# Performance work log

Measured on AMD Instinct MI355X. Metric: run time of the kernel, lower is better.

Reference implementation:

```python
import jax, jax.numpy as jnp
import numpy as np

EPS = 1e-6
N_HEADS, N_KV = 16, 4


def rmsnorm(x, w):
    return x * jax.lax.rsqrt(jnp.mean(x * x, axis=-1, keepdims=True) + EPS) * w


def setup_inputs() -> dict:
    key = jax.random.key(0)
    ks = jax.random.split(key, 9)
    B, T, D, F = 2, 2048, 2048, 8192
    KVD = N_KV * (D // N_HEADS)
    s = lambda k, shape, fan: (jax.random.normal(k, shape, jnp.float32) * (fan ** -0.5))
    return {
        "x": jax.random.normal(ks[0], (B, T, D), jnp.float32),
        "norm1_w": jnp.ones((D,), jnp.float32),
        "norm2_w": jnp.ones((D,), jnp.float32),
        "Wq": s(ks[1], (D, D), D),
        "Wk": s(ks[2], (D, KVD), D),
        "Wv": s(ks[3], (D, KVD), D),
        "Wo": s(ks[4], (D, D), D),
        "Wc": s(ks[5], (D, D), D),
        "W1": s(ks[6], (D, F), D),
        "W2": s(ks[7], (F, D), F),
        "W3": s(ks[8], (D, F), D),
    }


def reference(x, norm1_w, norm2_w, Wq, Wk, Wv, Wo, Wc, W1, W2, W3):
    B, T, D = x.shape
    dh = D // N_HEADS          # 128
    G = N_HEADS // N_KV        # groups per kv head
    scale = dh ** -0.5

    xn = rmsnorm(x, norm1_w)
    q = xn @ Wq                               # [B,T,D]
    pos = q @ Wc                              # CoPE stand-in: contextual positional bias on Q
    q = (q + pos).reshape(B, T, N_KV, G, dh)  # group q heads under their kv head
    k = (xn @ Wk).reshape(B, T, N_KV, dh)
    v = (xn @ Wv).reshape(B, T, N_KV, dh)

    # GQA without repeat_interleave: contract each group against shared K/V
    scores = jnp.einsum('bqkgd,bskd->bkgqs', q, k) * scale   # [B,KV,G,T,T]
    i = jnp.arange(T)
    causal = i[:, None] >= i[None, :]
    scores = jnp.where(causal, scores, -jnp.inf)
    w = jax.nn.softmax(scores, axis=-1)
    att = jnp.einsum('bkgqs,bskd->bqkgd', w, v).reshape(B, T, D)

    x = x + att @ Wo
    xn2 = rmsnorm(x, norm2_w)
    x = x + (jax.nn.silu(xn2 @ W1) * (xn2 @ W3)) @ W2
    return x
```

## Files before the change

### kernel.cpp

```cpp
#include <hip/hip_runtime.h>
#include <hip/hip_bf16.h>

typedef __attribute__((ext_vector_type(8))) short short8;
typedef __attribute__((ext_vector_type(4))) float floatx4;
typedef unsigned short ushort_t;

__device__ inline float b2f(ushort_t s) {
    return __uint_as_float(((unsigned int)s) << 16);
}
__device__ inline ushort_t f2b(float f) {
    unsigned int u = __float_as_uint(f);
    unsigned int r = 0x7fff + ((u >> 16) & 1);
    return (ushort_t)((u + r) >> 16);
}
__device__ inline void load8(const float* p, float* f) {
    float4 a = *(const float4*)p;
    float4 b = *(const float4*)(p + 4);
    f[0] = a.x; f[1] = a.y; f[2] = a.z; f[3] = a.w;
    f[4] = b.x; f[5] = b.y; f[6] = b.z; f[7] = b.w;
}
__device__ inline void gload16(const ushort_t* g, ushort_t* l) {
    __builtin_amdgcn_global_load_lds(
        (const __attribute__((address_space(1))) unsigned int*)g,
        (__attribute__((address_space(3))) unsigned int*)l, 16, 0, 0);
}

__global__ __launch_bounds__(256) void transpose_w(const float* __restrict__ src,
                                                   ushort_t* __restrict__ dst,
                                                   int K, int N) {
    __shared__ ushort_t tile[64][65];
    int kb = blockIdx.x * 64, nb = blockIdx.y * 64;
    int t = threadIdx.x;
#pragma unroll
    for (int i = 0; i < 4; ++i) {
        int r = (t >> 4) + i * 16;
        int c = (t & 15) * 4;
        float4 v = *(const float4*)(src + (size_t)(kb + r) * N + nb + c);
        tile[c + 0][r] = f2b(v.x);
        tile[c + 1][r] = f2b(v.y);
        tile[c + 2][r] = f2b(v.z);
        tile[c + 3][r] = f2b(v.w);
    }
    __syncthreads();
#pragma unroll
    for (int i = 0; i < 2; ++i) {
        int s = t + i * 256;
        int n = s >> 3, kc = (s & 7) * 8;
        ushort_t o[8];
#pragma unroll
        for (int j = 0; j < 8; ++j) o[j] = tile[n][kc + j];
        *(uint4*)(dst + (size_t)(nb + n) * K + kb + kc) = *(const uint4*)o;
    }
}

__global__ __launch_bounds__(256) void rmsnorm_kernel(const float* __restrict__ x,
                                                      const float* __restrict__ w,
                                                      ushort_t* __restrict__ out, int D) {
    int row = blockIdx.x;
    int t = threadIdx.x;
    const float* xr = x + (size_t)row * D;
    float f[8];
    load8(xr + t * 8, f);
    float ss = 0.f;
#pragma unroll
    for (int i = 0; i < 8; ++i) ss += f[i] * f[i];
#pragma unroll
    for (int m = 1; m < 64; m <<= 1) ss += __shfl_xor(ss, m);
    __shared__ float wsum[4];
    if ((t & 63) == 0) wsum[t >> 6] = ss;
    __syncthreads();
    float tot = wsum[0] + wsum[1] + wsum[2] + wsum[3];
    float r = rsqrtf(tot / (float)D + 1e-6f);
    float wf[8];
    load8(w + t * 8, wf);
    ushort_t o[8];
#pragma unroll
    for (int i = 0; i < 8; ++i) o[i] = f2b(f[i] * r * wf[i]);
    *(uint4*)(out + (size_t)row * D + t * 8) = *(const uint4*)o;
}

__global__ __launch_bounds__(256) void reduce_out(const ushort_t* __restrict__ p,
                                                  const float* __restrict__ resid,
                                                  float* __restrict__ out, int n) {
    int stride = gridDim.x * 256;
    for (int i = blockIdx.x * 256 + threadIdx.x; i * 8 < n; i += stride) {
        int i8 = i * 8;
        uint4 a = *(const uint4*)(p + i8);
        uint4 b = *(const uint4*)(p + n + i8);
        const ushort_t* ae = (const ushort_t*)&a;
        const ushort_t* be = (const ushort_t*)&b;
        float rr[8];
        load8(resid + i8, rr);
        float o[8];
#pragma unroll
        for (int j = 0; j < 8; ++j) o[j] = b2f(ae[j]) + b2f(be[j]) + rr[j];
        *(float4*)(out + i8) = make_float4(o[0], o[1], o[2], o[3]);
        *(float4*)(out + i8 + 4) = make_float4(o[4], o[5], o[6], o[7]);
    }
}

__device__ inline void vm6() { asm volatile("s_waitcnt vmcnt(6)" ::: "memory"); }

template <int MODE>
__global__ __launch_bounds__(512, 2) void gemm8(const ushort_t* __restrict__ A,
                                                const ushort_t* __restrict__ Bt,
                                                const ushort_t* __restrict__ aux,
                                                const float* __restrict__ aux2,
                                                void* __restrict__ Cv,
                                                void* __restrict__ C2v,
                                                void* __restrict__ C3v,
                                                int M, int N, int Ksub, int lda) {
    __shared__ __align__(16) ushort_t Lds[2 * 32768];
    const int tid = threadIdx.x;
    const int wv = tid >> 6, lane = tid & 63;
    const int l16 = lane & 15, l4 = lane >> 4;
    const int wr = wv >> 2, wc = wv & 3;
    int nwg = gridDim.x;
    int per = nwg >> 3;
    int wg = (blockIdx.x & 7) * per + (blockIdx.x >> 3);
    int mtiles = M >> 8;
    int bx = wg & (mtiles - 1);
    int by = wg / mtiles;
    int bm = bx << 8, bn = by << 8;
    int koff = blockIdx.y * Ksub;

    const int sr = tid >> 3;
    const int scol = (((tid & 7) ^ (sr & 7)) << 3);
    const ushort_t* gA = A + (size_t)(bm + sr) * lda + scol + koff;
    const ushort_t* gB = Bt + (size_t)(bn + sr) * lda + scol + koff;
    ushort_t* ldsw = Lds + wv * 512;

    const int ktiles = Ksub >> 6;
    const int niter = ktiles >> 1;
    const int km = ktiles - 1;

#define STG_A(slot, j, kt) gload16(gA + (size_t)((j) * 64) * lda + ((kt) << 6), ldsw + (slot) * 32768 + (j) * 4096)
#define STG_B(slot, j, kt) gload16(gB + (size_t)((j) * 64) * lda + ((kt) << 6), ldsw + (slot) * 32768 + 16384 + (j) * 4096)

    STG_A(0, 0, 0); STG_A(0, 2, 0); STG_A(0, 1, 0); STG_A(0, 3, 0);
    STG_B(0, 0, 0); STG_B(0, 1, 0); STG_B(0, 2, 0); STG_B(0, 3, 0);
    STG_A(1, 0, 1); STG_A(1, 2, 1);
    STG_B(1, 0, 1); STG_B(1, 1, 1); STG_B(1, 2, 1); STG_B(1, 3, 1);
    vm6();
    asm volatile("" ::: "memory");
    __builtin_amdgcn_s_barrier();

    const int lx = l4 ^ (l16 & 7);
    floatx4 acc[8][4] = {};
    short8 aR[4][2], bR[4][2];

#define DSA(slot, mh) { _Pragma("unroll") for (int m = 0; m < 4; ++m) { \
    _Pragma("unroll") for (int kk = 0; kk < 2; ++kk) \
      aR[m][kk] = *(const short8*)(Lds + (slot) * 32768 + \
          (wr * 128 + (mh) * 64 + m * 16 + l16) * 64 + ((lx ^ (kk << 2)) << 3)); } }
#define DSB(slot, nh) { _Pragma("unroll") for (int n = 0; n < 2; ++n) { \
    _Pragma("unroll") for (int kk = 0; kk < 2; ++kk) \
      bR[(nh) * 2 + n][kk] = *(const short8*)(Lds + (slot) * 32768 + 16384 + \
          (wc * 64 + ((nh) * 2 + n) * 16 + l16) * 64 + ((lx ^ (kk << 2)) << 3)); } }
#define QUAD(mh, nlo) { _Pragma("unroll") for (int m = 0; m < 4; ++m) \
    _Pragma("unroll") for (int n = 0; n < 2; ++n) \
    _Pragma("unroll") for (int kk = 0; kk < 2; ++kk) \
      acc[(mh) * 4 + m][(nlo) + n] = __builtin_amdgcn_mfma_f32_16x16x32_bf16( \
          aR[m][kk], bR[(nlo) + n][kk], acc[(mh) * 4 + m][(nlo) + n], 0, 0, 0); }
#define PHASE(DS, ST, MH, NLO, VM) { \
    DS; ST; \
    asm volatile("" ::: "memory"); \
    __builtin_amdgcn_s_barrier(); \
    asm volatile("s_waitcnt lgkmcnt(0)" ::: "memory"); \
    __builtin_amdgcn_sched_barrier(0); \
    __builtin_amdgcn_s_setprio(1); \
    QUAD(MH, NLO); \
    __builtin_amdgcn_s_setprio(0); \
    VM; \
    asm volatile("" ::: "memory"); \
    __builtin_amdgcn_s_barrier(); }

    for (int it = 0; it < niter; ++it) {
        int t1 = 2 * it + 1;
        int t2 = (2 * it + 2) & km;
        int t3 = (2 * it + 3) & km;
        PHASE({ DSA(0, 0); DSB(0, 0); }, { STG_A(1, 1, t1); STG_A(1, 3, t1); }, 0, 0, );
        PHASE({ DSB(0, 1); },            { STG_A(0, 0, t2); STG_A(0, 2, t2); }, 0, 2, );
        PHASE({ DSA(0, 1); },            { STG_B(0, 0, t2); STG_B(0, 1, t2); }, 1, 2, );
        PHASE({ },                       { STG_B(0, 2, t2); STG_B(0, 3, t2); }, 1, 0, vm6(); );
        PHASE({ DSA(1, 0); DSB(1, 0); }, { STG_A(0, 1, t2); STG_A(0, 3, t2); }, 0, 0, );
        PHASE({ DSB(1, 1); },            { STG_A(1, 0, t3); STG_A(1, 2, t3); }, 0, 2, );
        PHASE({ DSA(1, 1); },            { STG_B(1, 0, t3); STG_B(1, 1, t3); }, 1, 2, );
        PHASE({ },                       { STG_B(1, 2, t3); STG_B(1, 3, t3); }, 1, 0, vm6(); );
    }

#pragma unroll
    for (int mi = 0; mi < 8; ++mi)
#pragma unroll
        for (int ni = 0; ni < 4; ++ni)
#pragma unroll
            for (int r = 0; r < 4; ++r) {
                int row = bm + wr * 128 + mi * 16 + l4 * 4 + r;
                int col = bn + wc * 64 + ni * 16 + l16;
                size_t idx = (size_t)row * N + col;
                float v = acc[mi][ni][r];
                if (MODE == 0) {
                    ((ushort_t*)Cv)[idx] = f2b(v);
                } else if (MODE == 1) {
                    ((ushort_t*)Cv)[idx] = f2b(v + b2f(aux[idx]));
                } else if (MODE == 2) {
                    float h = b2f(aux[idx]);
                    ((ushort_t*)Cv)[idx] = f2b((h / (1.f + __expf(-h))) * v);
                } else if (MODE == 3) {
                    ((ushort_t*)Cv)[(size_t)blockIdx.y * M * N + idx] = f2b(v);
                } else if (MODE == 5) {
                    ((float*)Cv)[idx] = v + aux2[idx];
                } else if (MODE == 6) {
                    if (bn < 2048) {
                        ((ushort_t*)Cv)[(size_t)row * 2048 + col] = f2b(v);
                    } else if (bn < 2560) {
                        ((ushort_t*)C2v)[(size_t)row * 512 + (col - 2048)] = f2b(v);
                    } else {
                        ((ushort_t*)C3v)[(size_t)(col - 2560) * 4096 + row] = f2b(v);
                    }
                }
            }
#undef STG_A
#undef STG_B
#undef DSA
#undef DSB
#undef QUAD
#undef PHASE
}

#define QB 64
#define SB 64

__global__ __launch_bounds__(256, 2) void attn_kernel(const ushort_t* __restrict__ Q,
                                                      const ushort_t* __restrict__ Kb,
                                                      const ushort_t* __restrict__ VbT,
                                                      ushort_t* __restrict__ O, int Tlen) {
    const int D = 2048, KVD = 512, dh = 128;
    const int MTOK = 4096;
    int p = blockIdx.x, h = blockIdx.y, b = blockIdx.z;
    int kv = h >> 2;
    int t = threadIdx.x, wave = t >> 6, lane = t & 63;
    int l16 = lane & 15, l4 = lane >> 4;
    __shared__ __align__(16) ushort_t Ks[SB][dh + 8];
    __shared__ __align__(16) ushort_t Vt[dh][SB + 8];
    __shared__ __align__(16) ushort_t Ps[4][16][SB + 8];
    const float scale = 0.08838834764831845f;
    const ushort_t* Kg = Kb + ((size_t)(b * Tlen) + (t >> 4)) * KVD + kv * dh + (t & 15) * 8;
    const ushort_t* Vg = VbT + (size_t)(kv * dh + (t >> 3)) * MTOK + b * Tlen + (t & 7) * 8;

    for (int side = 0; side < 2; ++side) {
        int qt = side ? p : (31 - p);
        int qbase = qt * QB;
        int qfrag = qbase + wave * 16;
        short8 qf[4];
        const ushort_t* Qrow = Q + ((size_t)(b * Tlen) + qfrag + l16) * D + h * dh;
#pragma unroll
        for (int kk = 0; kk < 4; ++kk) qf[kk] = *(const short8*)(Qrow + kk * 32 + l4 * 8);
        floatx4 o_acc[8] = {};
        float m_r[4], l_r[4];
#pragma unroll
        for (int r = 0; r < 4; ++r) { m_r[r] = -INFINITY; l_r[r] = 0.f; }
        int nst = qt + 1;
        uint4 kreg[4], vreg[4];
#pragma unroll
        for (int p4 = 0; p4 < 4; ++p4) {
            kreg[p4] = *(const uint4*)(Kg + (size_t)(p4 * 16) * KVD);
            vreg[p4] = *(const uint4*)(Vg + (size_t)(p4 * 32) * MTOK);
        }
        for (int st = 0; st < nst; ++st) {
            __syncthreads();
#pragma unroll
            for (int p4 = 0; p4 < 4; ++p4) {
                *(uint4*)(&Ks[(t >> 4) + p4 * 16][(t & 15) * 8]) = kreg[p4];
                *(uint4*)(&Vt[(t >> 3) + p4 * 32][(t & 7) * 8]) = vreg[p4];
            }
            __syncthreads();
            if (st + 1 < nst) {
                size_t off = (size_t)(st + 1) * SB;
#pragma unroll
                for (int p4 = 0; p4 < 4; ++p4) {
                    kreg[p4] = *(const uint4*)(Kg + (off + p4 * 16) * KVD);
                    vreg[p4] = *(const uint4*)(Vg + (size_t)(p4 * 32) * MTOK + off);
                }
            }
            int s0 = st * SB;
            floatx4 sa[4] = {};
            __builtin_amdgcn_s_setprio(1);
#pragma unroll
            for (int ss = 0; ss < 4; ++ss)
#pragma unroll
                for (int kk = 0; kk < 4; ++kk) {
                    short8 kf = *(const short8*)(&Ks[ss * 16 + l16][kk * 32 + l4 * 8]);
                    sa[ss] = __builtin_amdgcn_mfma_f32_16x16x32_bf16(qf[kk], kf, sa[ss], 0, 0, 0);
                }
            __builtin_amdgcn_s_setprio(0);
            float sv[4][4], pmax[4];
#pragma unroll
            for (int r = 0; r < 4; ++r) pmax[r] = -INFINITY;
#pragma unroll
            for (int ss = 0; ss < 4; ++ss) {
                int scol = s0 + ss * 16 + l16;
#pragma unroll
                for (int r = 0; r < 4; ++r) {
                    int qrow = qfrag + l4 * 4 + r;
                    float v = sa[ss][r] * scale;
                    if (scol > qrow) v = -INFINITY;
                    sv[ss][r] = v;
                    pmax[r] = fmaxf(pmax[r], v);
                }
            }
#pragma unroll
            for (int m = 1; m < 16; m <<= 1)
#pragma unroll
                for (int r = 0; r < 4; ++r) pmax[r] = fmaxf(pmax[r], __shfl_xor(pmax[r], m));
            int cflag = 1;
#pragma unroll
            for (int r = 0; r < 4; ++r) cflag &= (pmax[r] <= m_r[r] + 8.f) ? 1 : 0;
            bool skip = __all(cflag);
            float mn[4], rsum[4];
#pragma unroll
            for (int r = 0; r < 4; ++r) {
                mn[r] = skip ? m_r[r] : fmaxf(m_r[r], pmax[r]);
                rsum[r] = 0.f;
            }
#pragma unroll
            for (int ss = 0; ss < 4; ++ss)
#pragma unroll
                for (int r = 0; r < 4; ++r) {
                    float pv = __expf(sv[ss][r] - mn[r]);
                    sv[ss][r] = pv;
                    rsum[r] += pv;
                }
#pragma unroll
            for (int m = 1; m < 16; m <<= 1)
#pragma unroll
                for (int r = 0; r < 4; ++r) rsum[r] += __shfl_xor(rsum[r], m);
            if (skip) {
#pragma unroll
                for (int r = 0; r < 4; ++r) l_r[r] += rsum[r];
            } else {
#pragma unroll
                for (int r = 0; r < 4; ++r) {
                    float esc = __expf(m_r[r] - mn[r]);
                    l_r[r] = l_r[r] * esc + rsum[r];
                    m_r[r] = mn[r];
#pragma unroll
                    for (int c = 0; c < 8; ++c) o_acc[c][r] *= esc;
                }
            }
#pragma unroll
            for (int ss = 0; ss < 4; ++ss)
#pragma unroll
                for (int r = 0; r < 4; ++r)
                    Ps[wave][l4 * 4 + r][ss * 16 + l16] = f2b(sv[ss][r]);
            short8 pa[2];
#pragma unroll
            for (int kk = 0; kk < 2; ++kk)
                pa[kk] = *(const short8*)(&Ps[wave][l16][kk * 32 + l4 * 8]);
            __builtin_amdgcn_s_setprio(1);
#pragma unroll
            for (int c = 0; c < 8; ++c)
#pragma unroll
                for (int kk = 0; kk < 2; ++kk) {
                    short8 vf = *(const short8*)(&Vt[c * 16 + l16][kk * 32 + l4 * 8]);
                    o_acc[c] = __builtin_amdgcn_mfma_f32_16x16x32_bf16(pa[kk], vf, o_acc[c], 0, 0, 0);
                }
            __builtin_amdgcn_s_setprio(0);
        }
#pragma unroll
        for (int c = 0; c < 8; ++c)
#pragma unroll
            for (int r = 0; r < 4; ++r) {
                int qrow = qfrag + l4 * 4 + r;
                int col = h * dh + c * 16 + l16;
                O[((size_t)(b * Tlen) + qrow) * D + col] = f2b(o_acc[c][r] / l_r[r]);
            }
    }
}

extern "C" void kernel_launch(void* const* d_in, const int* in_sizes, int n_in,
                              void* d_out, int out_size, void* d_ws, size_t ws_size,
                              hipStream_t stream) {
    const float* x   = (const float*)d_in[0];
    const float* n1w = (const float*)d_in[1];
    const float* n2w = (const float*)d_in[2];
    const float* Wq  = (const float*)d_in[3];
    const float* Wk  = (const float*)d_in[4];
    const float* Wv  = (const float*)d_in[5];
    const float* Wo  = (const float*)d_in[6];
    const float* Wc  = (const float*)d_in[7];
    const float* W1  = (const float*)d_in[8];
    const float* W2  = (const float*)d_in[9];
    const float* W3  = (const float*)d_in[10];
    float* out = (float*)d_out;

    const int B = 2, T = 2048, D = 2048, F = 8192, KVD = 512;
    const int M = B * T;
    const size_t XD   = (size_t)M * D * 2;
    const size_t XDF  = (size_t)M * D * 4;
    const size_t KVSZ = (size_t)M * KVD * 2;
    const size_t MF   = (size_t)M * F * 2;
    const size_t WDD  = (size_t)D * D * 2;
    const size_t WQKV = (size_t)(D + 2 * KVD) * D * 2;
    const size_t WDF  = (size_t)D * F * 2;

    char* w = (char*)d_ws;
    ushort_t* xn    = (ushort_t*)(w);
    ushort_t* qtmp  = (ushort_t*)(w + XD);
    ushort_t* qfin  = (ushort_t*)(w + 2 * XD);
    float*    x2f   = (float*)   (w + 3 * XD);
    ushort_t* kbuf  = (ushort_t*)(w + 3 * XD + XDF);
    ushort_t* vbufT = (ushort_t*)(w + 3 * XD + XDF + KVSZ);
    ushort_t* h1    = (ushort_t*)(w + 3 * XD + XDF + 2 * KVSZ);
    char* wt = w + 3 * XD + XDF + 2 * KVSZ + MF;
    ushort_t* WqkvT = (ushort_t*)(wt);
    ushort_t* WcT   = (ushort_t*)(wt + WQKV);
    ushort_t* WoT   = (ushort_t*)(wt + WQKV + WDD);
    ushort_t* W1T   = (ushort_t*)(wt + WQKV + 2 * WDD);
    ushort_t* W3T   = (ushort_t*)(wt + WQKV + 2 * WDD + WDF);
    ushort_t* W2T   = (ushort_t*)(wt + WQKV + 2 * WDD + 2 * WDF);

    dim3 blk(256);
    dim3 blk8(512);

    transpose_w<<<dim3(D / 64, D / 64), blk, 0, stream>>>(Wq, WqkvT, D, D);
    transpose_w<<<dim3(D / 64, KVD / 64), blk, 0, stream>>>(Wk, WqkvT + (size_t)2048 * D, D, KVD);
    transpose_w<<<dim3(D / 64, KVD / 64), blk, 0, stream>>>(Wv, WqkvT + (size_t)2560 * D, D, KVD);
    transpose_w<<<dim3(D / 64, D / 64), blk, 0, stream>>>(Wc, WcT, D, D);
    transpose_w<<<dim3(D / 64, D / 64), blk, 0, stream>>>(Wo, WoT, D, D);
    transpose_w<<<dim3(D / 64, F / 64), blk, 0, stream>>>(W1, W1T, D, F);
    transpose_w<<<dim3(D / 64, F / 64), blk, 0, stream>>>(W3, W3T, D, F);
    transpose_w<<<dim3(F / 64, D / 64), blk, 0, stream>>>(W2, W2T, F, D);

    rmsnorm_kernel<<<M, blk, 0, stream>>>(x, n1w, xn, D);
    gemm8<6><<<dim3((M / 256) * (3072 / 256)), blk8, 0, stream>>>(
        xn, WqkvT, nullptr, nullptr, qtmp, kbuf, vbufT, M, 3072, D, D);
    gemm8<1><<<dim3((M / 256) * (D / 256)), blk8, 0, stream>>>(
        qtmp, WcT, qtmp, nullptr, qfin, nullptr, nullptr, M, D, D, D);
    attn_kernel<<<dim3(16, 16, B), blk, 0, stream>>>(qfin, kbuf, vbufT, qtmp, T);
    gemm8<5><<<dim3((M / 256) * (D / 256)), blk8, 0, stream>>>(
        qtmp, WoT, nullptr, x, x2f, nullptr, nullptr, M, D, D, D);
    rmsnorm_kernel<<<M, blk, 0, stream>>>(x2f, n2w, xn, D);
    gemm8<0><<<dim3((M / 256) * (F / 256)), blk8, 0, stream>>>(
        xn, W1T, nullptr, nullptr, h1, nullptr, nullptr, M, F, D, D);
    gemm8<2><<<dim3((M / 256) * (F / 256)), blk8, 0, stream>>>(
        xn, W3T, h1, nullptr, h1, nullptr, nullptr, M, F, D, D);
    gemm8<3><<<dim3((M / 256) * (D / 256), 2), blk8, 0, stream>>>(
        h1, W2T, nullptr, nullptr, xn, nullptr, nullptr, M, D, F / 2, F);
    reduce_out<<<1024, blk, 0, stream>>>(xn, x2f, out, M * D);
}
```

Baseline: 876.1 us.

## Use 128x256 tile GEMM for D×D projections and stage attention output through LDS

Adds a gemm8h variant that uses 128-row by 256-column tiles with its own software-pipelined double-buffered schedule, and uses it for the Wc and Wo projections. The point is to launch twice as many workgroups (256 instead of 128) on the D×D GEMMs so more of the device's compute units stay busy. Separately, the attention kernel now writes its output tile into LDS first and then stores it to global memory in coalesced 16-byte chunks, replacing scattered 2-byte stores. The new kernel runs at one block per CU by its launch bounds and performs less data reuse per tile.

Measured after the change: 837.2 us. 4.4% less time.

```diff
diff --git a/kernel.cpp b/kernel.cpp
--- a/kernel.cpp
+++ b/kernel.cpp
@@ -100,6 +100,7 @@
 }
 
 __device__ inline void vm6() { asm volatile("s_waitcnt vmcnt(6)" ::: "memory"); }
+__device__ inline void vm4() { asm volatile("s_waitcnt vmcnt(4)" ::: "memory"); }
 
 template <int MODE>
 __global__ __launch_bounds__(512, 2) void gemm8(const ushort_t* __restrict__ A,
@@ -228,6 +229,112 @@
 #undef PHASE
 }
 
+template <int MODE>
+__global__ __launch_bounds__(512, 1) void gemm8h(const ushort_t* __restrict__ A,
+                                                 const ushort_t* __restrict__ Bt,
+                                                 const ushort_t* __restrict__ aux,
+                                                 const float* __restrict__ aux2,
+                                                 void* __restrict__ Cv,
+                                                 int M, int N, int K) {
+    __shared__ __align__(16) ushort_t Lds[2 * 24576];
+    const int tid = threadIdx.x;
+    const int wv = tid >> 6, lane = tid & 63;
+    const int l16 = lane & 15, l4 = lane >> 4;
+    const int wr = wv >> 2, wc = wv & 3;
+    int nwg = gridDim.x;
+    int per = nwg >> 3;
+    int wg = (blockIdx.x & 7) * per + (blockIdx.x >> 3);
+    int mtiles = M >> 7;
+    int bx = wg & (mtiles - 1);
+    int by = wg / mtiles;
+    int bm = bx << 7, bn = by << 8;
+
+    const int sr = tid >> 3;
+    const int scol = (((tid & 7) ^ (sr & 7)) << 3);
+    const ushort_t* gA = A + (size_t)(bm + sr) * K + scol;
+    const ushort_t* gB = Bt + (size_t)(bn + sr) * K + scol;
+    ushort_t* ldsw = Lds + wv * 512;
+
+    const int ktiles = K >> 6;
+    const int niter = ktiles >> 1;
+    const int km = ktiles - 1;
+
+#define HSTG_A(slot, j, kt) gload16(gA + (size_t)((j) * 64) * K + ((kt) << 6), ldsw + (slot) * 24576 + (j) * 4096)
+#define HSTG_B(slot, j, kt) gload16(gB + (size_t)((j) * 64) * K + ((kt) << 6), ldsw + (slot) * 24576 + 8192 + (j) * 4096)
+
+    HSTG_A(0, 0, 0); HSTG_A(0, 1, 0);
+    HSTG_B(0, 0, 0); HSTG_B(0, 1, 0); HSTG_B(0, 2, 0); HSTG_B(0, 3, 0);
+    HSTG_A(1, 0, 1); HSTG_A(1, 1, 1);
+    HSTG_B(1, 0, 1); HSTG_B(1, 1, 1);
+    vm4();
+    asm volatile("" ::: "memory");
+    __builtin_amdgcn_s_barrier();
+
+    const int lx = l4 ^ (l16 & 7);
+    floatx4 acc[4][4] = {};
+    short8 aR[2][2], bR[4][2];
+
+#define HDSA(slot, mh) { _Pragma("unroll") for (int m = 0; m < 2; ++m) { \
+    _Pragma("unroll") for (int kk = 0; kk < 2; ++kk) \
+      aR[m][kk] = *(const short8*)(Lds + (slot) * 24576 + \
+          (wr * 64 + (mh) * 32 + m * 16 + l16) * 64 + ((lx ^ (kk << 2)) << 3)); } }
+#define HDSB(slot, nh) { _Pragma("unroll") for (int n = 0; n < 2; ++n) { \
+    _Pragma("unroll") for (int kk = 0; kk < 2; ++kk) \
+      bR[(nh) * 2 + n][kk] = *(const short8*)(Lds + (slot) * 24576 + 8192 + \
+          (wc * 64 + ((nh) * 2 + n) * 16 + l16) * 64 + ((lx ^ (kk << 2)) << 3)); } }
+#define HQUAD(mh, nlo) { _Pragma("unroll") for (int m = 0; m < 2; ++m) \
+    _Pragma("unroll") for (int n = 0; n < 2; ++n) \
+    _Pragma("unroll") for (int kk = 0; kk < 2; ++kk) \
+      acc[(mh) * 2 + m][(nlo) + n] = __builtin_amdgcn_mfma_f32_16x16x32_bf16( \
+          aR[m][kk], bR[(nlo) + n][kk], acc[(mh) * 2 + m][(nlo) + n], 0, 0, 0); }
+#define HPHASE(DS, ST, MH, NLO, VM) { \
+    DS; ST; \
+    asm volatile("" ::: "memory"); \
+    __builtin_amdgcn_s_barrier(); \
+    asm volatile("s_waitcnt lgkmcnt(0)" ::: "memory"); \
+    __builtin_amdgcn_sched_barrier(0); \
+    __builtin_amdgcn_s_setprio(1); \
+    HQUAD(MH, NLO); \
+    __builtin_amdgcn_s_setprio(0); \
+    VM; \
+    asm volatile("" ::: "memory"); \
+    __builtin_amdgcn_s_barrier(); }
+
+    for (int it = 0; it < niter; ++it) {
+        int t1 = 2 * it + 1;
+        int t2 = (2 * it + 2) & km;
+        int t3 = (2 * it + 3) & km;
+        HPHASE({ HDSA(0, 0); HDSB(0, 0); }, { HSTG_B(1, 2, t1); HSTG_B(1, 3, t1); }, 0, 0, );
+        HPHASE({ HDSB(0, 1); },             { },                                     0, 2, );
+        HPHASE({ HDSA(0, 1); },             { HSTG_B(0, 0, t2); HSTG_B(0, 1, t2); }, 1, 2, );
+        HPHASE({ },                         { HSTG_B(0, 2, t2); HSTG_B(0, 3, t2); }, 1, 0, vm4(); );
+        HPHASE({ HDSA(1, 0); HDSB(1, 0); }, { HSTG_A(0, 0, t2); HSTG_A(0, 1, t2); }, 0, 0, );
+        HPHASE({ HDSB(1, 1); },             { },                                     0, 2, );
+        HPHASE({ HDSA(1, 1); },             { HSTG_B(1, 0, t3); HSTG_B(1, 1, t3); }, 1, 2, );
+        HPHASE({ },                         { HSTG_A(1, 0, t3); HSTG_A(1, 1, t3); }, 1, 0, vm4(); );
+    }
+
+#pragma unroll
+    for (int mi = 0; mi < 4; ++mi)
+#pragma unroll
+        for (int ni = 0; ni < 4; ++ni)
+#pragma unroll
+            for (int r = 0; r < 4; ++r) {
+                int row = bm + wr * 64 + mi * 16 + l4 * 4 + r;
+                int col = bn + wc * 64 + ni * 16 + l16;
+                size_t idx = (size_t)row * N + col;
+                float v = acc[mi][ni][r];
+                if (MODE == 1) ((ushort_t*)Cv)[idx] = f2b(v + b2f(aux[idx]));
+                else if (MODE == 5) ((float*)Cv)[idx] = v + aux2[idx];
+            }
+#undef HSTG_A
+#undef HSTG_B
+#undef HDSA
+#undef HDSB
+#undef HQUAD
+#undef HPHASE
+}
+
 #define QB 64
 #define SB 64
 
@@ -367,14 +474,22 @@
                 }
             __builtin_amdgcn_s_setprio(0);
         }
+        __syncthreads();
+        ushort_t* Osh = &Ks[0][0];
 #pragma unroll
         for (int c = 0; c < 8; ++c)
 #pragma unroll
-            for (int r = 0; r < 4; ++r) {
-                int qrow = qfrag + l4 * 4 + r;
-                int col = h * dh + c * 16 + l16;
-                O[((size_t)(b * Tlen) + qrow) * D + col] = f2b(o_acc[c][r] / l_r[r]);
-            }
+            for (int r = 0; r < 4; ++r)
+                Osh[(wave * 16 + l4 * 4 + r) * 136 + c * 16 + l16] = f2b(o_acc[c][r] / l_r[r]);
+        __syncthreads();
+        {
+            int orow = t >> 2, occ = (t & 3) * 32;
+            const ushort_t* srcp = Osh + orow * 136 + occ;
+            ushort_t* dstp = O + ((size_t)(b * Tlen) + qbase + orow) * D + h * dh + occ;
+#pragma unroll
+            for (int k = 0; k < 4; ++k)
+                *(uint4*)(dstp + k * 8) = *(const uint4*)(srcp + k * 8);
+        }
     }
 }
 
@@ -435,11 +550,11 @@
     rmsnorm_kernel<<<M, blk, 0, stream>>>(x, n1w, xn, D);
     gemm8<6><<<dim3((M / 256) * (3072 / 256)), blk8, 0, stream>>>(
         xn, WqkvT, nullptr, nullptr, qtmp, kbuf, vbufT, M, 3072, D, D);
-    gemm8<1><<<dim3((M / 256) * (D / 256)), blk8, 0, stream>>>(
-        qtmp, WcT, qtmp, nullptr, qfin, nullptr, nullptr, M, D, D, D);
+    gemm8h<1><<<dim3((M / 128) * (D / 256)), blk8, 0, stream>>>(
+        qtmp, WcT, qtmp, nullptr, qfin, M, D, D);
     attn_kernel<<<dim3(16, 16, B), blk, 0, stream>>>(qfin, kbuf, vbufT, qtmp, T);
-    gemm8<5><<<dim3((M / 256) * (D / 256)), blk8, 0, stream>>>(
-        qtmp, WoT, nullptr, x, x2f, nullptr, nullptr, M, D, D, D);
+    gemm8h<5><<<dim3((M / 128) * (D / 256)), blk8, 0, stream>>>(
+        qtmp, WoT, nullptr, x, x2f, M, D, D);
     rmsnorm_kernel<<<M, blk, 0, stream>>>(x2f, n2w, xn, D);
     gemm8<0><<<dim3((M / 256) * (F / 256)), blk8, 0, stream>>>(
         xn, W1T, nullptr, nullptr, h1, nullptr, nullptr, M, F, D, D);
```
